# Kernel optimization log

Measured on AMD Instinct MI355X. Metric: run time of the kernel, lower is better.

Reference implementation:

```python
import jax, jax.numpy as jnp
import numpy as np

N = 100000   # nodes
E = 1600000  # edges
G = 2048     # graphs
IN = 128     # in_channels
H = 128      # hidden_channels
L = 3        # num GIN layers


def setup_inputs() -> dict:
    key = jax.random.key(0)
    ks = jax.random.split(key, 16)
    s = 0.05
    rn = lambda k, shp: s * jax.random.normal(k, shp, dtype=jnp.float32)
    return {
        "x": jax.random.normal(ks[0], (N, IN), dtype=jnp.float32),
        "edge_index": jax.random.randint(ks[1], (2, E), 0, N, dtype=jnp.int32),
        "batch": jnp.sort(jax.random.randint(ks[2], (N,), 0, G, dtype=jnp.int32)),
        # encoder input projection
        "W_in": rn(ks[3], (IN, H)), "b_in": jnp.zeros((H,), jnp.float32),
        # GIN layers: MLP = Linear(H,H)-ReLU-Linear(H,H), learnable eps
        "Ws1": rn(ks[4], (L, H, H)), "bs1": jnp.zeros((L, H), jnp.float32),
        "Ws2": rn(ks[5], (L, H, H)), "bs2": jnp.zeros((L, H), jnp.float32),
        "eps": jnp.zeros((L,), jnp.float32),
        # encoder output projection (out_channels == hidden_channels)
        "W_out": rn(ks[6], (H, H)), "b_out": jnp.zeros((H,), jnp.float32),
        # decoder: Linear(H, H//2) - ReLU - Linear(H//2, IN)
        "Wd1": rn(ks[7], (H, H // 2)), "bd1": jnp.zeros((H // 2,), jnp.float32),
        "Wd2": rn(ks[8], (H // 2, IN)), "bd2": jnp.zeros((IN,), jnp.float32),
    }


def reference(x, edge_index, batch, W_in, b_in, Ws1, bs1, Ws2, bs2, eps,
              W_out, b_out, Wd1, bd1, Wd2, bd2):
    src, dst = edge_index[0], edge_index[1]
    # input projection
    h = jax.nn.relu(x @ W_in + b_in)                      # [N, H]
    # GIN message passing (sum aggregation)
    for l in range(L):
        agg = jax.ops.segment_sum(h[src], dst, num_segments=N)   # [N, H]
        z = (1.0 + eps[l]) * h + agg
        m = jax.nn.relu(z @ Ws1[l] + bs1[l]) @ Ws2[l] + bs2[l]
        h = jax.nn.relu(m)
    # global mean pool per graph
    pooled = jax.ops.segment_sum(h, batch, num_segments=G)       # [G, H]
    counts = jax.ops.segment_sum(jnp.ones((N,), h.dtype), batch, num_segments=G)
    pooled = pooled / jnp.maximum(counts, 1.0)[:, None]
    graph_embeddings = pooled @ W_out + b_out                    # [G, H]
    # gather graph embedding back to each node, then decode
    node_embeddings = graph_embeddings[batch]                    # [N, H]
    reconstructed = jax.nn.relu(node_embeddings @ Wd1 + bd1) @ Wd2 + bd2  # [N, IN]
    return reconstructed, graph_embeddings
```

## Files before the change

### kernel.cpp

```cpp
#include <hip/hip_runtime.h>

typedef unsigned int uint;
typedef unsigned short ushort;
typedef __attribute__((ext_vector_type(8))) short bf16x8;
typedef __attribute__((ext_vector_type(4))) float f32x4;
typedef __attribute__((ext_vector_type(4))) int int4v;

constexpr int N_ = 100000;
constexpr int E_ = 1600000;
constexpr int G_ = 2048;
constexpr int H_ = 128;
constexpr int WPSZ = 16384;
constexpr int NSLICE = 8;
constexpr int SL_SZ = N_ / NSLICE;
constexpr int SL_BLOCKS = 256;
constexpr int CAP = 64;
constexpr int CLDS = 136;

__device__ inline ushort f2bf(float f) {
    uint u = __builtin_bit_cast(uint, f);
    u += 0x7fffu + ((u >> 16) & 1u);
    return (ushort)(u >> 16);
}
__device__ inline float bflo(uint v) { return __builtin_bit_cast(float, v << 16); }
__device__ inline float bfhi(uint v) { return __builtin_bit_cast(float, v & 0xffff0000u); }

__global__ __launch_bounds__(256) void k_fill_c(const int* __restrict__ srcv, const int* __restrict__ dstv,
                                                int* __restrict__ cnt, int* __restrict__ csr_src) {
    int slice = blockIdx.x & (NSLICE - 1);
    int grp   = blockIdx.x >> 3;
    int lo = slice * SL_SZ, hi = lo + SL_SZ;
    int stride = SL_BLOCKS * 256;
    const int4v* d4 = (const int4v*)dstv;
    const int4v* s4 = (const int4v*)srcv;
    int nq = E_ / 4;
    for (int q = grp * 256 + threadIdx.x; q < nq; q += stride) {
        int4v d = __builtin_nontemporal_load(&d4[q]);
        int4v s = __builtin_nontemporal_load(&s4[q]);
        #pragma unroll
        for (int k = 0; k < 4; k++) {
            int dd = d[k];
            int ss = s[k];
            if (dd >= lo && dd < hi) {
                int slot = atomicAdd(&cnt[dd], 1);
                if (slot < CAP) csr_src[(size_t)dd * CAP + slot] = ss;
            }
        }
    }
}

__global__ __launch_bounds__(64) void k_pack(const float* __restrict__ W, ushort* __restrict__ Wp) {
    int lane = threadIdx.x;
    int n = ((blockIdx.x >> 2) * 16) + (lane & 15);
    int k0 = (blockIdx.x & 3) * 32 + (lane >> 4) * 8;
    bf16x8 v;
    #pragma unroll
    for (int j = 0; j < 8; j++) v[j] = (short)f2bf(W[(size_t)(k0 + j) * H_ + n]);
    *(bf16x8*)&Wp[(size_t)(blockIdx.x * 64 + lane) * 8] = v;
}

template <bool F32IN, bool RELU>
__global__ __launch_bounds__(256) void k_mm(const void* __restrict__ in, const ushort* __restrict__ Wp,
                                            const float* __restrict__ bias, ushort* __restrict__ out, int M) {
    __shared__ ushort sm[128 * CLDS];
    int t = threadIdx.x;
    #pragma unroll
    for (int i = 0; i < 8; i++) {
        int idx = i * 256 + t;
        *(bf16x8*)&sm[(size_t)idx * 8] = *(const bf16x8*)&Wp[(size_t)idx * 8];
    }
    __syncthreads();

    int wave = t >> 6, lane = t & 63;
    int col = lane & 15, kc = lane >> 4;
    int row0 = blockIdx.x * 128 + wave * 32;

    float bv[8];
    #pragma unroll
    for (int nt = 0; nt < 8; nt++) bv[nt] = bias[nt * 16 + col];

    f32x4 acc[2][8];
    #pragma unroll
    for (int rt = 0; rt < 2; rt++)
        #pragma unroll
        for (int nt = 0; nt < 8; nt++) {
            acc[rt][nt][0] = bv[nt]; acc[rt][nt][1] = bv[nt];
            acc[rt][nt][2] = bv[nt]; acc[rt][nt][3] = bv[nt];
        }

    #pragma unroll
    for (int kb = 0; kb < 4; kb++) {
        bf16x8 bf[8];
        #pragma unroll
        for (int nt = 0; nt < 8; nt++)
            bf[nt] = *(const bf16x8*)&sm[(size_t)(((nt * 4 + kb) * 64) + lane) * 8];
        #pragma unroll
        for (int rt = 0; rt < 2; rt++) {
            int r = row0 + rt * 16 + col;
            if (r > M - 1) r = M - 1;
            bf16x8 af;
            if (F32IN) {
                const float* fin = (const float*)in;
                float4 a0 = *(const float4*)&fin[(size_t)r * H_ + kb * 32 + kc * 8];
                float4 a1 = *(const float4*)&fin[(size_t)r * H_ + kb * 32 + kc * 8 + 4];
                af[0] = (short)f2bf(a0.x); af[1] = (short)f2bf(a0.y);
                af[2] = (short)f2bf(a0.z); af[3] = (short)f2bf(a0.w);
                af[4] = (short)f2bf(a1.x); af[5] = (short)f2bf(a1.y);
                af[6] = (short)f2bf(a1.z); af[7] = (short)f2bf(a1.w);
            } else {
                af = *(const bf16x8*)&((const ushort*)in)[(size_t)r * H_ + kb * 32 + kc * 8];
            }
            #pragma unroll
            for (int nt = 0; nt < 8; nt++)
                acc[rt][nt] = __builtin_amdgcn_mfma_f32_16x16x32_bf16(af, bf[nt], acc[rt][nt], 0, 0, 0);
        }
    }

    __syncthreads();
    #pragma unroll
    for (int rt = 0; rt < 2; rt++) {
        int rl0 = wave * 32 + rt * 16 + kc * 4;
        #pragma unroll
        for (int r = 0; r < 4; r++) {
            #pragma unroll
            for (int nt = 0; nt < 8; nt++) {
                float f = acc[rt][nt][r];
                if (RELU) f = fmaxf(f, 0.f);
                sm[(size_t)(rl0 + r) * CLDS + nt * 16 + col] = f2bf(f);
            }
        }
    }
    __syncthreads();

    int base_row = blockIdx.x * 128;
    #pragma unroll
    for (int i = 0; i < 8; i++) {
        int ch = i * 256 + t;
        int row = ch >> 4, part = ch & 15;
        if (base_row + row < M) {
            bf16x8 v = *(const bf16x8*)&sm[(size_t)row * CLDS + part * 8];
            *(bf16x8*)&out[(size_t)(base_row + row) * H_ + part * 8] = v;
        }
    }
}

__global__ __launch_bounds__(256) void k_agg(const uint* __restrict__ h, const int* __restrict__ cnt,
                                             const int* __restrict__ csr_src, const float* __restrict__ eps,
                                             int layer, uint* __restrict__ z) {
    int node = blockIdx.x * 4 + (threadIdx.x >> 6);
    int c = threadIdx.x & 63;
    int deg = cnt[node];
    if (deg > CAP) deg = CAP;
    const int* cs = csr_src + (size_t)node * CAP;
    float a0 = 0.f, a1 = 0.f;
    int j = 0;
    for (; j + 8 <= deg; j += 8) {
        int4v i0 = *(const int4v*)&cs[j];
        int4v i1 = *(const int4v*)&cs[j + 4];
        uint v0 = h[(size_t)i0[0] * 64 + c];
        uint v1 = h[(size_t)i0[1] * 64 + c];
        uint v2 = h[(size_t)i0[2] * 64 + c];
        uint v3 = h[(size_t)i0[3] * 64 + c];
        uint v4 = h[(size_t)i1[0] * 64 + c];
        uint v5 = h[(size_t)i1[1] * 64 + c];
        uint v6 = h[(size_t)i1[2] * 64 + c];
        uint v7 = h[(size_t)i1[3] * 64 + c];
        a0 += bflo(v0) + bflo(v1) + bflo(v2) + bflo(v3) + bflo(v4) + bflo(v5) + bflo(v6) + bflo(v7);
        a1 += bfhi(v0) + bfhi(v1) + bfhi(v2) + bfhi(v3) + bfhi(v4) + bfhi(v5) + bfhi(v6) + bfhi(v7);
    }
    for (; j + 4 <= deg; j += 4) {
        int4v i0 = *(const int4v*)&cs[j];
        uint v0 = h[(size_t)i0[0] * 64 + c];
        uint v1 = h[(size_t)i0[1] * 64 + c];
        uint v2 = h[(size_t)i0[2] * 64 + c];
        uint v3 = h[(size_t)i0[3] * 64 + c];
        a0 += bflo(v0) + bflo(v1) + bflo(v2) + bflo(v3);
        a1 += bfhi(v0) + bfhi(v1) + bfhi(v2) + bfhi(v3);
    }
    for (; j < deg; j++) {
        uint v = h[(size_t)cs[j] * 64 + c];
        a0 += bflo(v); a1 += bfhi(v);
    }
    float e1 = 1.0f + eps[layer];
    uint hv = h[(size_t)node * 64 + c];
    float o0 = fmaf(e1, bflo(hv), a0);
    float o1 = fmaf(e1, bfhi(hv), a1);
    z[(size_t)node * 64 + c] = (uint)f2bf(o0) | ((uint)f2bf(o1) << 16);
}

template <int KDIM, int NDIM, bool RELU>
__global__ __launch_bounds__(256) void k_lin(const float* __restrict__ in, const float* __restrict__ W,
                                             const float* __restrict__ bias, float* __restrict__ out) {
    constexpr int CV = NDIM / 4;
    constexpr int RPI = 256 / CV;
    constexpr int R = 4;
    constexpr int ROWS = RPI * R;
    __shared__ float4 Wl[KDIM * CV];
    for (int i = threadIdx.x; i < KDIM * CV; i += 256) Wl[i] = ((const float4*)W)[i];
    __syncthreads();

    int cv = threadIdx.x % CV;
    int rg = threadIdx.x / CV;
    int row0 = blockIdx.x * ROWS + rg * R;

    float4 bv = ((const float4*)bias)[cv];
    float4 acc[R];
    #pragma unroll
    for (int r = 0; r < R; r++) acc[r] = bv;

    const float4* in4 = (const float4*)in;
    #pragma unroll 2
    for (int k4 = 0; k4 < KDIM / 4; k4++) {
        float4 w0 = Wl[(4 * k4 + 0) * CV + cv];
        float4 w1 = Wl[(4 * k4 + 1) * CV + cv];
        float4 w2 = Wl[(4 * k4 + 2) * CV + cv];
        float4 w3 = Wl[(4 * k4 + 3) * CV + cv];
        #pragma unroll
        for (int r = 0; r < R; r++) {
            float4 a = in4[(size_t)(row0 + r) * (KDIM / 4) + k4];
            acc[r].x = fmaf(a.x, w0.x, fmaf(a.y, w1.x, fmaf(a.z, w2.x, fmaf(a.w, w3.x, acc[r].x))));
            acc[r].y = fmaf(a.x, w0.y, fmaf(a.y, w1.y, fmaf(a.z, w2.y, fmaf(a.w, w3.y, acc[r].y))));
            acc[r].z = fmaf(a.x, w0.z, fmaf(a.y, w1.z, fmaf(a.z, w2.z, fmaf(a.w, w3.z, acc[r].z))));
            acc[r].w = fmaf(a.x, w0.w, fmaf(a.y, w1.w, fmaf(a.z, w2.w, fmaf(a.w, w3.w, acc[r].w))));
        }
    }
    #pragma unroll
    for (int r = 0; r < R; r++) {
        float4 o = acc[r];
        if (RELU) {
            o.x = fmaxf(o.x, 0.f); o.y = fmaxf(o.y, 0.f);
            o.z = fmaxf(o.z, 0.f); o.w = fmaxf(o.w, 0.f);
        }
        ((float4*)out)[(size_t)(row0 + r) * CV + cv] = o;
    }
}

__global__ __launch_bounds__(64) void k_pool(const uint* __restrict__ h2, const int* __restrict__ batch,
                                             float* __restrict__ pooled, float* __restrict__ gcnt, int n) {
    int c = threadIdx.x;
    int base = blockIdx.x * 128;
    int nmax = min(base + 128, n);
    int gcur = batch[base];
    float a0 = 0.f, a1 = 0.f;
    int run = 0;
    for (int i = base; i < nmax; i++) {
        int g = batch[i];
        if (g != gcur) {
            atomicAdd(&pooled[(size_t)gcur * 128 + 2 * c], a0);
            atomicAdd(&pooled[(size_t)gcur * 128 + 2 * c + 1], a1);
            if (c == 0) atomicAdd(&gcnt[gcur], (float)run);
            a0 = 0.f; a1 = 0.f; run = 0; gcur = g;
        }
        uint v = h2[(size_t)i * 64 + c];
        a0 += bflo(v); a1 += bfhi(v);
        run++;
    }
    atomicAdd(&pooled[(size_t)gcur * 128 + 2 * c], a0);
    atomicAdd(&pooled[(size_t)gcur * 128 + 2 * c + 1], a1);
    if (c == 0) atomicAdd(&gcnt[gcur], (float)run);
}

__global__ __launch_bounds__(256) void k_div(float* __restrict__ pooled, const float* __restrict__ gcnt) {
    int i = blockIdx.x * 256 + threadIdx.x;
    float cnt = fmaxf(gcnt[i >> 7], 1.0f);
    pooled[i] = pooled[i] / cnt;
}

__global__ __launch_bounds__(256) void k_scatter(const float* __restrict__ recong, const int* __restrict__ batch,
                                                 float* __restrict__ out) {
    int i = blockIdx.x * 256 + threadIdx.x;
    int node = i >> 5;
    int c4 = i & 31;
    int g = batch[node];
    ((float4*)out)[(size_t)node * 32 + c4] = ((const float4*)recong)[(size_t)g * 32 + c4];
}


extern "C" void kernel_launch(void* const* d_in, const int* in_sizes, int n_in,
                              void* d_out, int out_size, void* d_ws, size_t ws_size,
                              hipStream_t stream) {
    const float* x     = (const float*)d_in[0];
    const int*   ei    = (const int*)d_in[1];
    const int*   batch = (const int*)d_in[2];
    const float* W_in  = (const float*)d_in[3];
    const float* b_in  = (const float*)d_in[4];
    const float* Ws1   = (const float*)d_in[5];
    const float* bs1   = (const float*)d_in[6];
    const float* Ws2   = (const float*)d_in[7];
    const float* bs2   = (const float*)d_in[8];
    const float* eps   = (const float*)d_in[9];
    const float* W_out = (const float*)d_in[10];
    const float* b_out = (const float*)d_in[11];
    const float* Wd1   = (const float*)d_in[12];
    const float* bd1   = (const float*)d_in[13];
    const float* Wd2   = (const float*)d_in[14];
    const float* bd2   = (const float*)d_in[15];

    const int* srcv = ei;
    const int* dstv = ei + E_;

    char* ws = (char*)d_ws;
    size_t off = 0;
    auto nextp = [&](size_t bytes) -> char* {
        char* p = ws + off;
        off += (bytes + 255) & ~(size_t)255;
        return p;
    };
    ushort* buf0    = (ushort*)nextp((size_t)N_ * H_ * 2);
    ushort* buf1    = (ushort*)nextp((size_t)N_ * H_ * 2);
    ushort* Wp      = (ushort*)nextp((size_t)7 * WPSZ * 2);
    int*   cnt      = (int*)nextp((size_t)N_ * 4);
    int*   csr_src  = (int*)nextp((size_t)N_ * CAP * 4);
    float* pooled   = (float*)nextp((size_t)G_ * H_ * 4);
    float* gcnt     = (float*)nextp((size_t)G_ * 4);
    float* tg       = (float*)nextp((size_t)G_ * 64 * 4);
    float* recong   = (float*)nextp((size_t)G_ * H_ * 4);

    float* out_recon = (float*)d_out;
    float* out_ge    = (float*)d_out + (size_t)N_ * H_;

    (void)hipMemsetAsync(cnt, 0, (size_t)N_ * 4, stream);
    (void)hipMemsetAsync(pooled, 0, (size_t)G_ * H_ * 4, stream);
    (void)hipMemsetAsync(gcnt, 0, (size_t)G_ * 4, stream);

    k_fill_c<<<NSLICE * SL_BLOCKS, 256, 0, stream>>>(srcv, dstv, cnt, csr_src);

    k_pack<<<32, 64, 0, stream>>>(W_in, Wp + 0 * WPSZ);
    for (int l = 0; l < 3; l++) {
        k_pack<<<32, 64, 0, stream>>>(Ws1 + (size_t)l * H_ * H_, Wp + (size_t)(1 + 2 * l) * WPSZ);
        k_pack<<<32, 64, 0, stream>>>(Ws2 + (size_t)l * H_ * H_, Wp + (size_t)(2 + 2 * l) * WPSZ);
    }

    int mmgrid = (N_ + 127) / 128;

    k_mm<true, true><<<mmgrid, 256, 0, stream>>>(x, Wp, b_in, buf0, N_);

    ushort* hb = buf0;
    ushort* ob = buf1;
    for (int l = 0; l < 3; l++) {
        k_agg<<<N_ / 4, 256, 0, stream>>>((const uint*)hb, cnt, csr_src, eps, l, (uint*)ob);
        k_mm<false, true><<<mmgrid, 256, 0, stream>>>(ob, Wp + (size_t)(1 + 2 * l) * WPSZ, bs1 + l * H_, hb, N_);
        k_mm<false, true><<<mmgrid, 256, 0, stream>>>(hb, Wp + (size_t)(2 + 2 * l) * WPSZ, bs2 + l * H_, ob, N_);
        ushort* tmp = hb; hb = ob; ob = tmp;
    }

    k_pool<<<(N_ + 127) / 128, 64, 0, stream>>>((const uint*)hb, batch, pooled, gcnt, N_);
    k_div<<<G_ * H_ / 256, 256, 0, stream>>>(pooled, gcnt);
    k_lin<128, 128, false><<<G_ / 32, 256, 0, stream>>>(pooled, W_out, b_out, out_ge);

    k_lin<128, 64, true><<<G_ / 64, 256, 0, stream>>>(out_ge, Wd1, bd1, tg);
    k_lin<64, 128, false><<<G_ / 32, 256, 0, stream>>>(tg, Wd2, bd2, recong);
    k_scatter<<<(size_t)N_ * 32 / 256, 256, 0, stream>>>(recong, batch, out_recon);
}
```

Baseline: 618.8 us.

## Fuse GIN MLP pair into one kernel, widen aggregation loads, batch setup kernels

The two per-layer MLP GEMMs are fused into one kernel, so the hidden activation stays in LDS instead of going through global memory. That kernel reads its weights directly from global memory rather than staging them in LDS. Aggregation now uses 32 lanes per node with 8-byte loads, and the three memsets and seven weight-pack launches are each merged into a single kernel. The LDS row padding also changes. Together these cut kernel launches and intermediate HBM traffic, at the cost of possible LDS bank conflicts from the new padding and more global weight reads per block.

New measurement: 551.4 us. 10.9% less time.

```diff
diff --git a/kernel.cpp b/kernel.cpp
--- a/kernel.cpp
+++ b/kernel.cpp
@@ -15,7 +15,7 @@
 constexpr int SL_SZ = N_ / NSLICE;
 constexpr int SL_BLOCKS = 256;
 constexpr int CAP = 64;
-constexpr int CLDS = 136;
+constexpr int CLDS = 132;
 
 __device__ inline ushort f2bf(float f) {
     uint u = __builtin_bit_cast(uint, f);
@@ -24,6 +24,14 @@
 }
 __device__ inline float bflo(uint v) { return __builtin_bit_cast(float, v << 16); }
 __device__ inline float bfhi(uint v) { return __builtin_bit_cast(float, v & 0xffff0000u); }
+
+__global__ __launch_bounds__(256) void k_zero(int* __restrict__ cnt, float* __restrict__ pooled,
+                                              float* __restrict__ gcnt) {
+    int i = blockIdx.x * 256 + threadIdx.x;
+    if (i < N_) cnt[i] = 0;
+    else if (i < N_ + G_ * H_) pooled[i - N_] = 0.f;
+    else if (i < N_ + G_ * H_ + G_) gcnt[i - N_ - G_ * H_] = 0.f;
+}
 
 __global__ __launch_bounds__(256) void k_fill_c(const int* __restrict__ srcv, const int* __restrict__ dstv,
                                                 int* __restrict__ cnt, int* __restrict__ csr_src) {
@@ -49,19 +57,27 @@
     }
 }
 
-__global__ __launch_bounds__(64) void k_pack(const float* __restrict__ W, ushort* __restrict__ Wp) {
+__global__ __launch_bounds__(64) void k_pack_all(const float* __restrict__ W_in, const float* __restrict__ Ws1,
+                                                 const float* __restrict__ Ws2, ushort* __restrict__ Wp) {
+    int m = blockIdx.x >> 5;
+    int sub = blockIdx.x & 31;
+    const float* W;
+    if (m == 0) W = W_in;
+    else if (m & 1) W = Ws1 + (size_t)((m - 1) >> 1) * H_ * H_;
+    else W = Ws2 + (size_t)((m >> 1) - 1) * H_ * H_;
+    ushort* dst = Wp + (size_t)m * WPSZ;
+
     int lane = threadIdx.x;
-    int n = ((blockIdx.x >> 2) * 16) + (lane & 15);
-    int k0 = (blockIdx.x & 3) * 32 + (lane >> 4) * 8;
+    int n = ((sub >> 2) * 16) + (lane & 15);
+    int k0 = (sub & 3) * 32 + (lane >> 4) * 8;
     bf16x8 v;
     #pragma unroll
     for (int j = 0; j < 8; j++) v[j] = (short)f2bf(W[(size_t)(k0 + j) * H_ + n]);
-    *(bf16x8*)&Wp[(size_t)(blockIdx.x * 64 + lane) * 8] = v;
-}
-
-template <bool F32IN, bool RELU>
-__global__ __launch_bounds__(256) void k_mm(const void* __restrict__ in, const ushort* __restrict__ Wp,
-                                            const float* __restrict__ bias, ushort* __restrict__ out, int M) {
+    *(bf16x8*)&dst[(size_t)(sub * 64 + lane) * 8] = v;
+}
+
+__global__ __launch_bounds__(256) void k_mm_in(const float* __restrict__ in, const ushort* __restrict__ Wp,
+                                               const float* __restrict__ bias, ushort* __restrict__ out, int M) {
     __shared__ ushort sm[128 * CLDS];
     int t = threadIdx.x;
     #pragma unroll
@@ -98,18 +114,13 @@
         for (int rt = 0; rt < 2; rt++) {
             int r = row0 + rt * 16 + col;
             if (r > M - 1) r = M - 1;
+            float4 a0 = *(const float4*)&in[(size_t)r * H_ + kb * 32 + kc * 8];
+            float4 a1 = *(const float4*)&in[(size_t)r * H_ + kb * 32 + kc * 8 + 4];
             bf16x8 af;
-            if (F32IN) {
-                const float* fin = (const float*)in;
-                float4 a0 = *(const float4*)&fin[(size_t)r * H_ + kb * 32 + kc * 8];
-                float4 a1 = *(const float4*)&fin[(size_t)r * H_ + kb * 32 + kc * 8 + 4];
-                af[0] = (short)f2bf(a0.x); af[1] = (short)f2bf(a0.y);
-                af[2] = (short)f2bf(a0.z); af[3] = (short)f2bf(a0.w);
-                af[4] = (short)f2bf(a1.x); af[5] = (short)f2bf(a1.y);
-                af[6] = (short)f2bf(a1.z); af[7] = (short)f2bf(a1.w);
-            } else {
-                af = *(const bf16x8*)&((const ushort*)in)[(size_t)r * H_ + kb * 32 + kc * 8];
-            }
+            af[0] = (short)f2bf(a0.x); af[1] = (short)f2bf(a0.y);
+            af[2] = (short)f2bf(a0.z); af[3] = (short)f2bf(a0.w);
+            af[4] = (short)f2bf(a1.x); af[5] = (short)f2bf(a1.y);
+            af[6] = (short)f2bf(a1.z); af[7] = (short)f2bf(a1.w);
             #pragma unroll
             for (int nt = 0; nt < 8; nt++)
                 acc[rt][nt] = __builtin_amdgcn_mfma_f32_16x16x32_bf16(af, bf[nt], acc[rt][nt], 0, 0, 0);
@@ -121,14 +132,10 @@
     for (int rt = 0; rt < 2; rt++) {
         int rl0 = wave * 32 + rt * 16 + kc * 4;
         #pragma unroll
-        for (int r = 0; r < 4; r++) {
-            #pragma unroll
-            for (int nt = 0; nt < 8; nt++) {
-                float f = acc[rt][nt][r];
-                if (RELU) f = fmaxf(f, 0.f);
-                sm[(size_t)(rl0 + r) * CLDS + nt * 16 + col] = f2bf(f);
-            }
-        }
+        for (int r = 0; r < 4; r++)
+            #pragma unroll
+            for (int nt = 0; nt < 8; nt++)
+                sm[(size_t)(rl0 + r) * CLDS + nt * 16 + col] = f2bf(fmaxf(acc[rt][nt][r], 0.f));
     }
     __syncthreads();
 
@@ -137,55 +144,149 @@
     for (int i = 0; i < 8; i++) {
         int ch = i * 256 + t;
         int row = ch >> 4, part = ch & 15;
-        if (base_row + row < M) {
-            bf16x8 v = *(const bf16x8*)&sm[(size_t)row * CLDS + part * 8];
-            *(bf16x8*)&out[(size_t)(base_row + row) * H_ + part * 8] = v;
-        }
-    }
-}
-
-__global__ __launch_bounds__(256) void k_agg(const uint* __restrict__ h, const int* __restrict__ cnt,
+        if (base_row + row < M)
+            *(bf16x8*)&out[(size_t)(base_row + row) * H_ + part * 8] =
+                *(const bf16x8*)&sm[(size_t)row * CLDS + part * 8];
+    }
+}
+
+__global__ __launch_bounds__(256) void k_mlp(const ushort* __restrict__ in,
+                                             const ushort* __restrict__ Wp1, const float* __restrict__ b1,
+                                             const ushort* __restrict__ Wp2, const float* __restrict__ b2,
+                                             ushort* __restrict__ out, int M) {
+    __shared__ ushort sm[128 * CLDS];
+    int t = threadIdx.x;
+    int wave = t >> 6, lane = t & 63;
+    int col = lane & 15, kc = lane >> 4;
+    int row0 = blockIdx.x * 128 + wave * 32;
+
+    f32x4 acc[2][8];
+    #pragma unroll
+    for (int nt = 0; nt < 8; nt++) {
+        float b = b1[nt * 16 + col];
+        #pragma unroll
+        for (int rt = 0; rt < 2; rt++) {
+            acc[rt][nt][0] = b; acc[rt][nt][1] = b;
+            acc[rt][nt][2] = b; acc[rt][nt][3] = b;
+        }
+    }
+    #pragma unroll
+    for (int kb = 0; kb < 4; kb++) {
+        bf16x8 bf[8];
+        #pragma unroll
+        for (int nt = 0; nt < 8; nt++)
+            bf[nt] = *(const bf16x8*)&Wp1[(size_t)(((nt * 4 + kb) * 64) + lane) * 8];
+        #pragma unroll
+        for (int rt = 0; rt < 2; rt++) {
+            int r = row0 + rt * 16 + col;
+            if (r > M - 1) r = M - 1;
+            bf16x8 af = *(const bf16x8*)&in[(size_t)r * H_ + kb * 32 + kc * 8];
+            #pragma unroll
+            for (int nt = 0; nt < 8; nt++)
+                acc[rt][nt] = __builtin_amdgcn_mfma_f32_16x16x32_bf16(af, bf[nt], acc[rt][nt], 0, 0, 0);
+        }
+    }
+    #pragma unroll
+    for (int rt = 0; rt < 2; rt++) {
+        int rl0 = wave * 32 + rt * 16 + kc * 4;
+        #pragma unroll
+        for (int r = 0; r < 4; r++)
+            #pragma unroll
+            for (int nt = 0; nt < 8; nt++)
+                sm[(size_t)(rl0 + r) * CLDS + nt * 16 + col] = f2bf(fmaxf(acc[rt][nt][r], 0.f));
+    }
+    __syncthreads();
+
+    #pragma unroll
+    for (int nt = 0; nt < 8; nt++) {
+        float b = b2[nt * 16 + col];
+        #pragma unroll
+        for (int rt = 0; rt < 2; rt++) {
+            acc[rt][nt][0] = b; acc[rt][nt][1] = b;
+            acc[rt][nt][2] = b; acc[rt][nt][3] = b;
+        }
+    }
+    #pragma unroll
+    for (int kb = 0; kb < 4; kb++) {
+        bf16x8 bf[8];
+        #pragma unroll
+        for (int nt = 0; nt < 8; nt++)
+            bf[nt] = *(const bf16x8*)&Wp2[(size_t)(((nt * 4 + kb) * 64) + lane) * 8];
+        #pragma unroll
+        for (int rt = 0; rt < 2; rt++) {
+            bf16x8 af = *(const bf16x8*)&sm[(size_t)(wave * 32 + rt * 16 + col) * CLDS + kb * 32 + kc * 8];
+            #pragma unroll
+            for (int nt = 0; nt < 8; nt++)
+                acc[rt][nt] = __builtin_amdgcn_mfma_f32_16x16x32_bf16(af, bf[nt], acc[rt][nt], 0, 0, 0);
+        }
+    }
+    #pragma unroll
+    for (int rt = 0; rt < 2; rt++) {
+        int rl0 = wave * 32 + rt * 16 + kc * 4;
+        #pragma unroll
+        for (int r = 0; r < 4; r++)
+            #pragma unroll
+            for (int nt = 0; nt < 8; nt++)
+                sm[(size_t)(rl0 + r) * CLDS + nt * 16 + col] = f2bf(fmaxf(acc[rt][nt][r], 0.f));
+    }
+    #pragma unroll
+    for (int i = 0; i < 8; i++) {
+        int ch = i * 64 + lane;
+        int row = wave * 32 + (ch >> 4);
+        int part = ch & 15;
+        int grow = blockIdx.x * 128 + row;
+        if (grow < M)
+            *(bf16x8*)&out[(size_t)grow * H_ + part * 8] =
+                *(const bf16x8*)&sm[(size_t)row * CLDS + part * 8];
+    }
+}
+
+__global__ __launch_bounds__(256) void k_agg(const uint2* __restrict__ h, const int* __restrict__ cnt,
                                              const int* __restrict__ csr_src, const float* __restrict__ eps,
-                                             int layer, uint* __restrict__ z) {
-    int node = blockIdx.x * 4 + (threadIdx.x >> 6);
-    int c = threadIdx.x & 63;
+                                             int layer, uint2* __restrict__ z) {
+    int node = blockIdx.x * 8 + (threadIdx.x >> 5);
+    int c = threadIdx.x & 31;
     int deg = cnt[node];
     if (deg > CAP) deg = CAP;
     const int* cs = csr_src + (size_t)node * CAP;
-    float a0 = 0.f, a1 = 0.f;
+    float a0 = 0.f, a1 = 0.f, a2 = 0.f, a3 = 0.f;
     int j = 0;
     for (; j + 8 <= deg; j += 8) {
         int4v i0 = *(const int4v*)&cs[j];
         int4v i1 = *(const int4v*)&cs[j + 4];
-        uint v0 = h[(size_t)i0[0] * 64 + c];
-        uint v1 = h[(size_t)i0[1] * 64 + c];
-        uint v2 = h[(size_t)i0[2] * 64 + c];
-        uint v3 = h[(size_t)i0[3] * 64 + c];
-        uint v4 = h[(size_t)i1[0] * 64 + c];
-        uint v5 = h[(size_t)i1[1] * 64 + c];
-        uint v6 = h[(size_t)i1[2] * 64 + c];
-        uint v7 = h[(size_t)i1[3] * 64 + c];
-        a0 += bflo(v0) + bflo(v1) + bflo(v2) + bflo(v3) + bflo(v4) + bflo(v5) + bflo(v6) + bflo(v7);
-        a1 += bfhi(v0) + bfhi(v1) + bfhi(v2) + bfhi(v3) + bfhi(v4) + bfhi(v5) + bfhi(v6) + bfhi(v7);
+        #pragma unroll
+        for (int k = 0; k < 4; k++) {
+            uint2 v = h[(size_t)i0[k] * 32 + c];
+            a0 += bflo(v.x); a1 += bfhi(v.x); a2 += bflo(v.y); a3 += bfhi(v.y);
+        }
+        #pragma unroll
+        for (int k = 0; k < 4; k++) {
+            uint2 v = h[(size_t)i1[k] * 32 + c];
+            a0 += bflo(v.x); a1 += bfhi(v.x); a2 += bflo(v.y); a3 += bfhi(v.y);
+        }
     }
     for (; j + 4 <= deg; j += 4) {
         int4v i0 = *(const int4v*)&cs[j];
-        uint v0 = h[(size_t)i0[0] * 64 + c];
-        uint v1 = h[(size_t)i0[1] * 64 + c];
-        uint v2 = h[(size_t)i0[2] * 64 + c];
-        uint v3 = h[(size_t)i0[3] * 64 + c];
-        a0 += bflo(v0) + bflo(v1) + bflo(v2) + bflo(v3);
-        a1 += bfhi(v0) + bfhi(v1) + bfhi(v2) + bfhi(v3);
+        #pragma unroll
+        for (int k = 0; k < 4; k++) {
+            uint2 v = h[(size_t)i0[k] * 32 + c];
+            a0 += bflo(v.x); a1 += bfhi(v.x); a2 += bflo(v.y); a3 += bfhi(v.y);
+        }
     }
     for (; j < deg; j++) {
-        uint v = h[(size_t)cs[j] * 64 + c];
-        a0 += bflo(v); a1 += bfhi(v);
+        uint2 v = h[(size_t)cs[j] * 32 + c];
+        a0 += bflo(v.x); a1 += bfhi(v.x); a2 += bflo(v.y); a3 += bfhi(v.y);
     }
     float e1 = 1.0f + eps[layer];
-    uint hv = h[(size_t)node * 64 + c];
-    float o0 = fmaf(e1, bflo(hv), a0);
-    float o1 = fmaf(e1, bfhi(hv), a1);
-    z[(size_t)node * 64 + c] = (uint)f2bf(o0) | ((uint)f2bf(o1) << 16);
+    uint2 hv = h[(size_t)node * 32 + c];
+    float o0 = fmaf(e1, bflo(hv.x), a0);
+    float o1 = fmaf(e1, bfhi(hv.x), a1);
+    float o2 = fmaf(e1, bflo(hv.y), a2);
+    float o3 = fmaf(e1, bfhi(hv.y), a3);
+    uint2 ov;
+    ov.x = (uint)f2bf(o0) | ((uint)f2bf(o1) << 16);
+    ov.y = (uint)f2bf(o2) | ((uint)f2bf(o3) << 16);
+    z[(size_t)node * 32 + c] = ov;
 }
 
 template <int KDIM, int NDIM, bool RELU>
@@ -319,32 +420,26 @@
     float* out_recon = (float*)d_out;
     float* out_ge    = (float*)d_out + (size_t)N_ * H_;
 
-    (void)hipMemsetAsync(cnt, 0, (size_t)N_ * 4, stream);
-    (void)hipMemsetAsync(pooled, 0, (size_t)G_ * H_ * 4, stream);
-    (void)hipMemsetAsync(gcnt, 0, (size_t)G_ * 4, stream);
+    int zgrid = (N_ + G_ * H_ + G_ + 255) / 256;
+    k_zero<<<zgrid, 256, 0, stream>>>(cnt, pooled, gcnt);
 
     k_fill_c<<<NSLICE * SL_BLOCKS, 256, 0, stream>>>(srcv, dstv, cnt, csr_src);
 
-    k_pack<<<32, 64, 0, stream>>>(W_in, Wp + 0 * WPSZ);
+    k_pack_all<<<7 * 32, 64, 0, stream>>>(W_in, Ws1, Ws2, Wp);
+
+    int mmgrid = (N_ + 127) / 128;
+
+    k_mm_in<<<mmgrid, 256, 0, stream>>>(x, Wp, b_in, buf0, N_);
+
     for (int l = 0; l < 3; l++) {
-        k_pack<<<32, 64, 0, stream>>>(Ws1 + (size_t)l * H_ * H_, Wp + (size_t)(1 + 2 * l) * WPSZ);
-        k_pack<<<32, 64, 0, stream>>>(Ws2 + (size_t)l * H_ * H_, Wp + (size_t)(2 + 2 * l) * WPSZ);
-    }
-
-    int mmgrid = (N_ + 127) / 128;
-
-    k_mm<true, true><<<mmgrid, 256, 0, stream>>>(x, Wp, b_in, buf0, N_);
-
-    ushort* hb = buf0;
-    ushort* ob = buf1;
-    for (int l = 0; l < 3; l++) {
-        k_agg<<<N_ / 4, 256, 0, stream>>>((const uint*)hb, cnt, csr_src, eps, l, (uint*)ob);
-        k_mm<false, true><<<mmgrid, 256, 0, stream>>>(ob, Wp + (size_t)(1 + 2 * l) * WPSZ, bs1 + l * H_, hb, N_);
-        k_mm<false, true><<<mmgrid, 256, 0, stream>>>(hb, Wp + (size_t)(2 + 2 * l) * WPSZ, bs2 + l * H_, ob, N_);
-        ushort* tmp = hb; hb = ob; ob = tmp;
-    }
-
-    k_pool<<<(N_ + 127) / 128, 64, 0, stream>>>((const uint*)hb, batch, pooled, gcnt, N_);
+        k_agg<<<N_ / 8, 256, 0, stream>>>((const uint2*)buf0, cnt, csr_src, eps, l, (uint2*)buf1);
+        k_mlp<<<mmgrid, 256, 0, stream>>>(buf1,
+                                          Wp + (size_t)(1 + 2 * l) * WPSZ, bs1 + l * H_,
+                                          Wp + (size_t)(2 + 2 * l) * WPSZ, bs2 + l * H_,
+                                          buf0, N_);
+    }
+
+    k_pool<<<(N_ + 127) / 128, 64, 0, stream>>>((const uint*)buf0, batch, pooled, gcnt, N_);
     k_div<<<G_ * H_ / 256, 256, 0, stream>>>(pooled, gcnt);
     k_lin<128, 128, false><<<G_ / 32, 256, 0, stream>>>(pooled, W_out, b_out, out_ge);
 
```
